# Performance work log

Measured on AMD Instinct MI355X. Metric: run time of the kernel, lower is better.

## Reference

```python
import jax, jax.numpy as jnp
import numpy as np

S, D, H, E = 4096, 1024, 16, 64  # seq_len, embed_dim, n_heads, head_size


def setup_inputs() -> dict:
    key = jax.random.key(0)
    ks = jax.random.split(key, 8)
    s_d = 1.0 / np.sqrt(D).astype(np.float32)
    return {
        "x": jax.random.normal(ks[0], (S, D), jnp.float32),
        # per-head Q/K/V projections (no bias), stacked over heads: [H, D, E]
        "Wk": jax.random.normal(ks[1], (H, D, E), jnp.float32) * s_d,
        "Wq": jax.random.normal(ks[2], (H, D, E), jnp.float32) * s_d,
        "Wv": jax.random.normal(ks[3], (H, D, E), jnp.float32) * s_d,
        # output projection Dense(D) with bias
        "Wo": jax.random.normal(ks[4], (H * E, D), jnp.float32) * (1.0 / np.sqrt(H * E).astype(np.float32)),
        "bo": jnp.zeros((D,), jnp.float32),
        # MLP: Dense(4D) -> gelu -> Dense(D), both with bias
        "W1": jax.random.normal(ks[5], (D, 4 * D), jnp.float32) * s_d,
        "b1": jnp.zeros((4 * D,), jnp.float32),
        "W2": jax.random.normal(ks[6], (4 * D, D), jnp.float32) * (1.0 / np.sqrt(4 * D).astype(np.float32)),
        "b2": jnp.zeros((D,), jnp.float32),
    }


def _attention(x, Wk, Wq, Wv):
    # per-head projections, vectorized over heads (original loops in Python)
    k = jnp.einsum('sd,hde->hse', x, Wk)
    q = jnp.einsum('sd,hde->hse', x, Wq)
    v = jnp.einsum('sd,hde->hse', x, Wv)
    # NOTE: original computes keys @ queries.T -> scores[i, j] = k_i . q_j
    scores = jnp.einsum('hse,hte->hst', k, q) / jnp.sqrt(jnp.float32(E))
    mask = jnp.tril(jnp.ones((x.shape[0], x.shape[0]), dtype=bool))  # [S, S]
    w = jax.nn.softmax(jnp.where(mask, scores, -jnp.inf), axis=-1)   # [H, S, S]
    out = jnp.einsum('hst,hte->hse', w, v)                            # [H, S, E]
    # concatenate heads along feature axis (head 0 first, matching the loop)
    return out.transpose(1, 0, 2).reshape(x.shape[0], -1)             # [S, H*E]


def reference(x, Wk, Wq, Wv, Wo, bo, W1, b1, W2, b2):
    x = x + _attention(x, Wk, Wq, Wv) @ Wo + bo
    h = jax.nn.gelu(x @ W1 + b1, approximate=True)  # flax default gelu (tanh approx)
    return x + h @ W2 + b2
```

## Files before the change

kernel.cpp:

```cpp
#include <hip/hip_runtime.h>

typedef __attribute__((ext_vector_type(8))) short s16x8;
typedef __attribute__((ext_vector_type(4))) short s16x4;
typedef __attribute__((ext_vector_type(4))) float f32x4;


__device__ __forceinline__ unsigned short f2bf(float f) {
    union { float f; unsigned u; } v; v.f = f;
    unsigned r = v.u + 0x7FFFu + ((v.u >> 16) & 1u);
    return (unsigned short)(r >> 16);
}

__device__ __forceinline__ float bf2f(unsigned short b) {
    union { unsigned u; float f; } v; v.u = ((unsigned)b) << 16;
    return v.f;
}

__device__ __forceinline__ unsigned cvt_pk_bf16(float lo, float hi) {
    unsigned r;
    asm("v_cvt_pk_bf16_f32 %0, %1, %2" : "=v"(r) : "v"(lo), "v"(hi));
    return r;
}

__device__ __forceinline__ float exp2_fast(float x) {
    float r;
    asm("v_exp_f32 %0, %1" : "=v"(r) : "v"(x));
    return r;
}

__device__ __forceinline__ float gelu_tanh(float x) {
    float u = 0.7978845608028654f * (x + 0.044715f * x * x * x);
    float au = fabsf(u);
    float t = 1.f - 2.f / (__expf(2.f * au) + 1.f);
    t = (u < 0.f) ? -t : t;
    return 0.5f * x * (1.f + t);
}

__device__ __forceinline__ void load_lds16(const void* g, void* l) {
    __builtin_amdgcn_global_load_lds(
        (const __attribute__((address_space(1))) void*)g,
        (__attribute__((address_space(3))) void*)l, 16, 0, 0);
}

__device__ __forceinline__ void xcd_remap(int& bx, int& by) {
    const int gx = gridDim.x;
    const int nwg = gx * gridDim.y;
    const int id = by * gx + bx;
    const int nid = (id & 7) * (nwg >> 3) + (id >> 3);
    bx = nid % gx; by = nid / gx;
}


__global__ void convert_bf16_k(const float* __restrict__ in,
                               unsigned short* __restrict__ out, int n) {
    int i = (blockIdx.x * blockDim.x + threadIdx.x) * 4;
    if (i >= n) return;
    float4 v = *(const float4*)(in + i);
    ushort4 o;
    o.x = f2bf(v.x); o.y = f2bf(v.y); o.z = f2bf(v.z); o.w = f2bf(v.w);
    *(ushort4*)(out + i) = o;
}

__global__ void transpose_k(const float* __restrict__ in,
                            unsigned short* __restrict__ out, int R, int C) {
    __shared__ float tile[32][33];
    const int b = blockIdx.z;
    const int c0 = blockIdx.x * 32, r0 = blockIdx.y * 32;
    const float* inb = in + (size_t)b * R * C;
    unsigned short* outb = out + (size_t)b * R * C;
    const int tx = threadIdx.x, ty = threadIdx.y;
    #pragma unroll
    for (int i = 0; i < 4; ++i)
        tile[ty + i*8][tx] = inb[(size_t)(r0 + ty + i*8) * C + c0 + tx];
    __syncthreads();
    #pragma unroll
    for (int i = 0; i < 4; ++i)
        outb[(size_t)(c0 + ty + i*8) * R + r0 + tx] = f2bf(tile[tx][ty + i*8]);
}

template<int EPI>
__global__ __launch_bounds__(256) void gemm_bt(
    const unsigned short* __restrict__ A,
    const unsigned short* __restrict__ BT,
    const float* __restrict__ bias,
    const float* __restrict__ resid,
    float* __restrict__ Cf,
    unsigned short* __restrict__ Cb,
    int M, int N, int K)
{
    __shared__ unsigned short As[3][128 * 32];
    __shared__ unsigned short Bs[3][128 * 32];
    const int tid = threadIdx.x;
    const int w  = tid >> 6, l = tid & 63;
    const int wr = w >> 1,  wc = w & 1;
    const int lg = l >> 4,  ll = l & 15;
    int bx = blockIdx.x, by = blockIdx.y;
    xcd_remap(bx, by);
    const int m0 = by * 128, n0 = bx * 128;

    const int srow = w * 16 + (l >> 2);
    const int scol = (((l & 3) ^ ((l >> 2) & 3))) * 8;

    f32x4 acc[4][4] = {};

    auto stage = [&](int buf, int k0) {
        #pragma unroll
        for (int i = 0; i < 2; ++i) {
            load_lds16(A  + (size_t)(m0 + srow + i*64) * K + k0 + scol,
                       (char*)As[buf] + i*4096 + w*1024);
            load_lds16(BT + (size_t)(n0 + srow + i*64) * K + k0 + scol,
                       (char*)Bs[buf] + i*4096 + w*1024);
        }
    };

    const int nsteps = K >> 5;
    stage(0, 0); stage(1, 32);
    int buf = 0;
    for (int s = 0; s < nsteps; ++s) {
        if (s + 1 < nsteps) asm volatile("s_waitcnt vmcnt(4)" ::: "memory");
        else                asm volatile("s_waitcnt vmcnt(0)" ::: "memory");
        __builtin_amdgcn_s_barrier();
        s16x8 a[4], b[4];
        #pragma unroll
        for (int m = 0; m < 4; ++m) {
            const int row = wr*64 + m*16 + ll;
            a[m] = *(const s16x8*)&As[buf][row * 32 + ((lg ^ (ll & 3)) * 8)];
        }
        #pragma unroll
        for (int n = 0; n < 4; ++n) {
            const int row = wc*64 + n*16 + ll;
            b[n] = *(const s16x8*)&Bs[buf][row * 32 + ((lg ^ (ll & 3)) * 8)];
        }
        int bnext = buf + 2; if (bnext >= 3) bnext -= 3;
        if (s + 2 < nsteps) stage(bnext, (s + 2) << 5);
        __builtin_amdgcn_s_setprio(1);
        #pragma unroll
        for (int m = 0; m < 4; ++m)
            #pragma unroll
            for (int n = 0; n < 4; ++n)
                acc[m][n] = __builtin_amdgcn_mfma_f32_16x16x32_bf16(a[m], b[n], acc[m][n], 0, 0, 0);
        __builtin_amdgcn_s_setprio(0);
        buf = (buf == 2) ? 0 : buf + 1;
    }

    #pragma unroll
    for (int m = 0; m < 4; ++m) {
        #pragma unroll
        for (int n = 0; n < 4; ++n) {
            const int col = n0 + wc*64 + n*16 + ll;
            #pragma unroll
            for (int r = 0; r < 4; ++r) {
                const int row = m0 + wr*64 + m*16 + lg*4 + r;
                float v = acc[m][n][r];
                if constexpr (EPI == 2) v = gelu_tanh(v + bias[col]);
                if constexpr (EPI == 4) v *= (col < 1024) ? 0.1803368801f : 1.0f;
                Cb[(size_t)row * N + col] = f2bf(v);
            }
        }
    }
}

template<int EPI>
__global__ __launch_bounds__(256) void gemm_bt64(
    const unsigned short* __restrict__ A,
    const unsigned short* __restrict__ BT,
    const float* __restrict__ bias,
    const float* __restrict__ resid,
    float* __restrict__ Cf,
    unsigned short* __restrict__ Cb,
    int M, int N, int K)
{
    __shared__ unsigned short As[4][128 * 32];
    __shared__ unsigned short Bs[4][64 * 32];
    const int tid = threadIdx.x;
    const int w  = tid >> 6, l = tid & 63;
    const int lg = l >> 4,  ll = l & 15;
    int bx = blockIdx.x, by = blockIdx.y;
    xcd_remap(bx, by);
    const int m0 = by * 128, n0 = bx * 64;

    const int srowA = w * 16 + (l >> 2);
    const int scolA = (((l & 3) ^ ((l >> 2) & 3))) * 8;
    const int srowB = tid >> 2;
    const int scolB = (((tid & 3) ^ ((tid >> 2) & 3))) * 8;

    f32x4 acc[2][4] = {};

    auto stage = [&](int buf, int k0) {
        #pragma unroll
        for (int i = 0; i < 2; ++i)
            load_lds16(A + (size_t)(m0 + srowA + i*64) * K + k0 + scolA,
                       (char*)As[buf] + i*4096 + w*1024);
        load_lds16(BT + (size_t)(n0 + srowB) * K + k0 + scolB,
                   (char*)Bs[buf] + w*1024);
    };

    const int nsteps = K >> 5;
    stage(0, 0); stage(1, 32); stage(2, 64);
    int buf = 0;
    for (int s = 0; s < nsteps; ++s) {
        const int rem = nsteps - 1 - s;
        if (rem >= 2)      asm volatile("s_waitcnt vmcnt(6)" ::: "memory");
        else if (rem == 1) asm volatile("s_waitcnt vmcnt(3)" ::: "memory");
        else               asm volatile("s_waitcnt vmcnt(0)" ::: "memory");
        __builtin_amdgcn_s_barrier();
        s16x8 a[2], b[4];
        #pragma unroll
        for (int m = 0; m < 2; ++m) {
            const int row = w*32 + m*16 + ll;
            a[m] = *(const s16x8*)&As[buf][row * 32 + ((lg ^ (ll & 3)) * 8)];
        }
        #pragma unroll
        for (int n = 0; n < 4; ++n) {
            const int row = n*16 + ll;
            b[n] = *(const s16x8*)&Bs[buf][row * 32 + ((lg ^ (ll & 3)) * 8)];
        }
        int bnext = buf + 3; if (bnext >= 4) bnext -= 4;
        if (s + 3 < nsteps) stage(bnext, (s + 3) << 5);
        __builtin_amdgcn_s_setprio(1);
        #pragma unroll
        for (int m = 0; m < 2; ++m)
            #pragma unroll
            for (int n = 0; n < 4; ++n)
                acc[m][n] = __builtin_amdgcn_mfma_f32_16x16x32_bf16(a[m], b[n], acc[m][n], 0, 0, 0);
        __builtin_amdgcn_s_setprio(0);
        buf = (buf + 1) & 3;
    }

    #pragma unroll
    for (int m = 0; m < 2; ++m) {
        #pragma unroll
        for (int n = 0; n < 4; ++n) {
            const int col = n0 + n*16 + ll;
            #pragma unroll
            for (int r = 0; r < 4; ++r) {
                const int row = m0 + w*32 + m*16 + lg*4 + r;
                float v = acc[m][n][r];
                if constexpr (EPI == 1 || EPI == 3) v += bias[col] + resid[(size_t)row * N + col];
                if constexpr (EPI != 3)
                    Cb[(size_t)row * N + col] = f2bf(v);
                if constexpr (EPI == 1 || EPI == 3)
                    Cf[(size_t)row * N + col] = v;
            }
        }
    }
}

__global__ __launch_bounds__(256) void attn_k(
    const unsigned short* __restrict__ Rq,
    const unsigned short* __restrict__ Ck,
    const unsigned short* __restrict__ Vt,
    unsigned short* __restrict__ Ppart,
    float* __restrict__ Lpart)
{
    __shared__ unsigned short Ks[3][64 * 64];
    __shared__ unsigned short Vs[3][64 * 64];

    const int bx = blockIdx.x;
    const int h  = bx & 15;
    const int j  = (bx >> 4) & 1;
    const int sb = 31 - (bx >> 5);
    const int t0 = j ? (sb + 1) : 0;
    const int t1 = j ? (2*sb + 2) : (sb + 1);

    const int tid = threadIdx.x;
    const int w = tid >> 6, l = tid & 63;
    const int lg = l >> 4, ll = l & 15;

    const int gsrc  = ((l & 7) ^ (l >> 3)) * 8;
    const int kOff0 = (w*16 +     (l >> 3)) * 2048 + h*64 + gsrc;
    const int kOff1 = (w*16 + 8 + (l >> 3)) * 2048 + h*64 + gsrc;
    const int vOff0 = (h*64 + w*16 +     (l >> 3)) * 4096 + gsrc;
    const int vOff1 = (h*64 + w*16 + 8 + (l >> 3)) * 4096 + gsrc;
    const int ldsOff = w * 2048;

    int qkoff[4][2];
    #pragma unroll
    for (int jj = 0; jj < 4; ++jj) {
        const int row = jj*16 + ll, r7 = row & 7;
        qkoff[jj][0] = row*128 + ((lg)     ^ r7) * 16;
        qkoff[jj][1] = row*128 + ((4 + lg) ^ r7) * 16;
    }
    int pvoff[4][2][2];
    #pragma unroll
    for (int n = 0; n < 4; ++n) {
        const int row = n*16 + ll, r7 = row & 7;
        #pragma unroll
        for (int c = 0; c < 2; ++c) {
            const int gl = (c*4     + (lg >> 1)) ^ r7;
            const int gh = (c*4 + 2 + (lg >> 1)) ^ r7;
            pvoff[n][c][0] = row*128 + gl*16 + (lg & 1)*8;
            pvoff[n][c][1] = row*128 + gh*16 + (lg & 1)*8;
        }
    }

    auto stage = [&](int t, int buf) {
        const unsigned short* qsrc = Ck + (size_t)t * 131072;
        const unsigned short* vsrc = Vt + t * 64;
        char* kd = (char*)Ks[buf] + ldsOff;
        char* vd = (char*)Vs[buf] + ldsOff;
        load_lds16(qsrc + kOff0, kd);
        load_lds16(qsrc + kOff1, kd + 1024);
        load_lds16(vsrc + vOff0, vd);
        load_lds16(vsrc + vOff1, vd + 1024);
    };

    const int row0 = sb*128 + w*32;
    const int qgA  = row0 + ll;
    const int qgB  = row0 + 16 + ll;
    const size_t rbA = (size_t)qgA * 2048 + h*64;
    const size_t rbB = (size_t)qgB * 2048 + h*64;
    const s16x8 rA0 = *(const s16x8*)&Rq[rbA + lg*8];
    const s16x8 rA1 = *(const s16x8*)&Rq[rbA + 32 + lg*8];
    const s16x8 rB0 = *(const s16x8*)&Rq[rbB + lg*8];
    const s16x8 rB1 = *(const s16x8*)&Rq[rbB + 32 + lg*8];

    const short onebf = (short)0x3F80;
    const s16x8 ones = {onebf, onebf, onebf, onebf, onebf, onebf, onebf, onebf};

    f32x4 o[2][4] = {};
    f32x4 o4[2] = {};

    stage(t0, 0);
    if (t0 + 1 < t1) stage(t0 + 1, 1);
    int buf = 0;

    for (int t = t0; t < t1; ++t) {
        if (t < t1-1) asm volatile("s_waitcnt vmcnt(4)" ::: "memory");
        else          asm volatile("s_waitcnt vmcnt(0)" ::: "memory");
        __builtin_amdgcn_s_barrier();
        const char* kb = (const char*)Ks[buf];
        const char* vb = (const char*)Vs[buf];
        const bool diag = (t >= 2*sb);

        f32x4 st[2][4];
        __builtin_amdgcn_s_setprio(1);
        #pragma unroll
        for (int jj = 0; jj < 4; ++jj) {
            s16x8 k0 = *(const s16x8*)(kb + qkoff[jj][0]);
            s16x8 k1 = *(const s16x8*)(kb + qkoff[jj][1]);
            f32x4 z = {0.f, 0.f, 0.f, 0.f};
            f32x4 ta = __builtin_amdgcn_mfma_f32_16x16x32_bf16(k0, rA0, z, 0, 0, 0);
            st[0][jj] = __builtin_amdgcn_mfma_f32_16x16x32_bf16(k1, rA1, ta, 0, 0, 0);
            f32x4 tb = __builtin_amdgcn_mfma_f32_16x16x32_bf16(k0, rB0, z, 0, 0, 0);
            st[1][jj] = __builtin_amdgcn_mfma_f32_16x16x32_bf16(k1, rB1, tb, 0, 0, 0);
        }
        __builtin_amdgcn_s_setprio(0);

        int bnext = buf + 2; if (bnext >= 3) bnext -= 3;
        if (t + 2 < t1) stage(t + 2, bnext);

        float p[2][4][4];
        if (diag) {
            #pragma unroll
            for (int jj = 0; jj < 4; ++jj)
                #pragma unroll
                for (int r = 0; r < 4; ++r) {
                    const int jg = t*64 + jj*16 + lg*4 + r;
                    p[0][jj][r] = exp2_fast((jg > qgA) ? -3e38f : st[0][jj][r]);
                    p[1][jj][r] = exp2_fast((jg > qgB) ? -3e38f : st[1][jj][r]);
                }
        } else {
            #pragma unroll
            for (int rs = 0; rs < 2; ++rs)
                #pragma unroll
                for (int jj = 0; jj < 4; ++jj)
                    #pragma unroll
                    for (int r = 0; r < 4; ++r)
                        p[rs][jj][r] = exp2_fast(st[rs][jj][r]);
        }

        s16x8 apv[2][2];
        #pragma unroll
        for (int rs = 0; rs < 2; ++rs)
            #pragma unroll
            for (int c = 0; c < 2; ++c) {
                union { unsigned u[4]; s16x8 v; } pk;
                pk.u[0] = cvt_pk_bf16(p[rs][2*c][0],   p[rs][2*c][1]);
                pk.u[1] = cvt_pk_bf16(p[rs][2*c][2],   p[rs][2*c][3]);
                pk.u[2] = cvt_pk_bf16(p[rs][2*c+1][0], p[rs][2*c+1][1]);
                pk.u[3] = cvt_pk_bf16(p[rs][2*c+1][2], p[rs][2*c+1][3]);
                apv[rs][c] = pk.v;
            }
        __builtin_amdgcn_s_setprio(1);
        #pragma unroll
        for (int rs = 0; rs < 2; ++rs) {
            o4[rs] = __builtin_amdgcn_mfma_f32_16x16x32_bf16(apv[rs][0], ones, o4[rs], 0, 0, 0);
            o4[rs] = __builtin_amdgcn_mfma_f32_16x16x32_bf16(apv[rs][1], ones, o4[rs], 0, 0, 0);
        }
        #pragma unroll
        for (int n = 0; n < 4; ++n) {
            #pragma unroll
            for (int c = 0; c < 2; ++c) {
                s16x4 lo = *(const s16x4*)(vb + pvoff[n][c][0]);
                s16x4 hi = *(const s16x4*)(vb + pvoff[n][c][1]);
                union { s16x4 h2[2]; s16x8 v; } u;
                u.h2[0] = lo; u.h2[1] = hi;
                o[0][n] = __builtin_amdgcn_mfma_f32_16x16x32_bf16(apv[0][c], u.v, o[0][n], 0, 0, 0);
                o[1][n] = __builtin_amdgcn_mfma_f32_16x16x32_bf16(apv[1][c], u.v, o[1][n], 0, 0, 0);
            }
        }
        __builtin_amdgcn_s_setprio(0);

        buf = (buf == 2) ? 0 : buf + 1;
    }

    unsigned short* Pout = Ppart + (size_t)j * 4194304;
    float* Lout = Lpart + (size_t)j * 65536;
    #pragma unroll
    for (int rs = 0; rs < 2; ++rs)
        #pragma unroll
        for (int r = 0; r < 4; ++r) {
            const int row = row0 + rs*16 + lg*4 + r;
            const size_t orow = (size_t)row * 1024 + h * 64;
            #pragma unroll
            for (int n = 0; n < 4; ++n)
                Pout[orow + n*16 + ll] = f2bf(o[rs][n][r]);
            if (ll == 0) Lout[row * 16 + h] = o4[rs][r];
        }
}

__global__ __launch_bounds__(256) void attn_combine_k(
    const unsigned short* __restrict__ P,
    const float* __restrict__ L,
    unsigned short* __restrict__ Out)
{
    const int idx = (blockIdx.x * 256 + threadIdx.x) * 4;
    const int row = idx >> 10, h = (idx & 1023) >> 6;
    const float inv = 1.f / (L[row*16 + h] + L[65536 + row*16 + h]);
    ushort4 a = *(const ushort4*)(P + idx);
    ushort4 b = *(const ushort4*)(P + 4194304 + idx);
    ushort4 o;
    o.x = f2bf((bf2f(a.x) + bf2f(b.x)) * inv);
    o.y = f2bf((bf2f(a.y) + bf2f(b.y)) * inv);
    o.z = f2bf((bf2f(a.z) + bf2f(b.z)) * inv);
    o.w = f2bf((bf2f(a.w) + bf2f(b.w)) * inv);
    *(ushort4*)(Out + idx) = o;
}


extern "C" void kernel_launch(void* const* d_in, const int* in_sizes, int n_in,
                              void* d_out, int out_size, void* d_ws, size_t ws_size,
                              hipStream_t stream) {
    const float* x  = (const float*)d_in[0];
    const float* Wk = (const float*)d_in[1];
    const float* Wq = (const float*)d_in[2];
    const float* Wv = (const float*)d_in[3];
    const float* Wo = (const float*)d_in[4];
    const float* bo = (const float*)d_in[5];
    const float* W1 = (const float*)d_in[6];
    const float* b1 = (const float*)d_in[7];
    const float* W2 = (const float*)d_in[8];
    const float* b2 = (const float*)d_in[9];
    float* out = (float*)d_out;

    char* ws = (char*)d_ws;
    unsigned short* x_bf  = (unsigned short*)(ws);
    unsigned short* WqkT  = (unsigned short*)(ws + (8u  << 20));
    unsigned short* WvT   = (unsigned short*)(ws + (12u << 20));
    unsigned short* WoT   = (unsigned short*)(ws + (14u << 20));
    unsigned short* W1T   = (unsigned short*)(ws + (16u << 20));
    unsigned short* W2T   = (unsigned short*)(ws + (24u << 20));
    unsigned short* QKm   = (unsigned short*)(ws + (32u << 20));
    unsigned short* attn  = (unsigned short*)(ws + (48u << 20));
    unsigned short* Vt    = (unsigned short*)(ws + (56u << 20));
    float*          yf    = (float*)(ws + (64u << 20));
    float*          Lpart = (float*)ws;
    unsigned short* Ppart = (unsigned short*)(ws + (64u << 20));
    unsigned short* y_bf  = x_bf;
    unsigned short* h_bf  = QKm;

    dim3 tb(32, 8);
    convert_bf16_k<<<4096, 256, 0, stream>>>(x, x_bf, 4096 * 1024);
    transpose_k<<<dim3(2, 32, 16),  tb, 0, stream>>>(Wq, WqkT,               1024, 64);
    transpose_k<<<dim3(2, 32, 16),  tb, 0, stream>>>(Wk, WqkT + 1024 * 1024, 1024, 64);
    transpose_k<<<dim3(2, 32, 16),  tb, 0, stream>>>(Wv, WvT, 1024, 64);
    transpose_k<<<dim3(32, 32, 1),  tb, 0, stream>>>(Wo, WoT, 1024, 1024);
    transpose_k<<<dim3(128, 32, 1), tb, 0, stream>>>(W1, W1T, 1024, 4096);
    transpose_k<<<dim3(32, 128, 1), tb, 0, stream>>>(W2, W2T, 4096, 1024);

    gemm_bt<4><<<dim3(16, 32), 256, 0, stream>>>(x_bf, WqkT, nullptr, nullptr, nullptr,
                                                 QKm, 4096, 2048, 1024);
    gemm_bt64<0><<<dim3(64, 8), 256, 0, stream>>>(WvT, x_bf, nullptr, nullptr, nullptr,
                                                  Vt, 1024, 4096, 1024);

    attn_k<<<1024, 256, 0, stream>>>(QKm + 1024 , QKm , Vt, Ppart, Lpart);
    attn_combine_k<<<4096, 256, 0, stream>>>(Ppart, Lpart, attn);

    gemm_bt64<1><<<dim3(16, 32), 256, 0, stream>>>(attn, WoT, bo, x, yf, y_bf, 4096, 1024, 1024);
    gemm_bt<2><<<dim3(32, 32),   256, 0, stream>>>(y_bf, W1T, b1, nullptr, nullptr, h_bf, 4096, 4096, 1024);
    gemm_bt64<3><<<dim3(16, 32), 256, 0, stream>>>(h_bf, W2T, b2, yf, out, nullptr, 4096, 1024, 4096);
}
```

Measured before the change: 251.8 us.

## Split-K the second MLP GEMM with 128x128 tiles plus a combine kernel

```diff
diff --git a/kernel.cpp b/kernel.cpp
--- a/kernel.cpp
+++ b/kernel.cpp
@@ -86,7 +86,7 @@
     const float* __restrict__ resid,
     float* __restrict__ Cf,
     unsigned short* __restrict__ Cb,
-    int M, int N, int K)
+    int M, int N, int K, int klen)
 {
     __shared__ unsigned short As[3][128 * 32];
     __shared__ unsigned short Bs[3][128 * 32];
@@ -97,6 +97,7 @@
     int bx = blockIdx.x, by = blockIdx.y;
     xcd_remap(bx, by);
     const int m0 = by * 128, n0 = bx * 128;
+    const int koff = (EPI == 5) ? (int)blockIdx.z * klen : 0;
 
     const int srow = w * 16 + (l >> 2);
     const int scol = (((l & 3) ^ ((l >> 2) & 3))) * 8;
@@ -106,14 +107,14 @@
     auto stage = [&](int buf, int k0) {
         #pragma unroll
         for (int i = 0; i < 2; ++i) {
-            load_lds16(A  + (size_t)(m0 + srow + i*64) * K + k0 + scol,
+            load_lds16(A  + (size_t)(m0 + srow + i*64) * K + koff + k0 + scol,
                        (char*)As[buf] + i*4096 + w*1024);
-            load_lds16(BT + (size_t)(n0 + srow + i*64) * K + k0 + scol,
+            load_lds16(BT + (size_t)(n0 + srow + i*64) * K + koff + k0 + scol,
                        (char*)Bs[buf] + i*4096 + w*1024);
         }
     };
 
-    const int nsteps = K >> 5;
+    const int nsteps = ((EPI == 5) ? klen : K) >> 5;
     stage(0, 0); stage(1, 32);
     int buf = 0;
     for (int s = 0; s < nsteps; ++s) {
@@ -143,6 +144,7 @@
         buf = (buf == 2) ? 0 : buf + 1;
     }
 
+    unsigned short* Cbz = (EPI == 5) ? (Cb + (size_t)blockIdx.z * M * N) : Cb;
     #pragma unroll
     for (int m = 0; m < 4; ++m) {
         #pragma unroll
@@ -154,7 +156,7 @@
                 float v = acc[m][n][r];
                 if constexpr (EPI == 2) v = gelu_tanh(v + bias[col]);
                 if constexpr (EPI == 4) v *= (col < 1024) ? 0.1803368801f : 1.0f;
-                Cb[(size_t)row * N + col] = f2bf(v);
+                Cbz[(size_t)row * N + col] = f2bf(v);
             }
         }
     }
@@ -236,14 +238,32 @@
             for (int r = 0; r < 4; ++r) {
                 const int row = m0 + w*32 + m*16 + lg*4 + r;
                 float v = acc[m][n][r];
-                if constexpr (EPI == 1 || EPI == 3) v += bias[col] + resid[(size_t)row * N + col];
-                if constexpr (EPI != 3)
-                    Cb[(size_t)row * N + col] = f2bf(v);
-                if constexpr (EPI == 1 || EPI == 3)
+                if constexpr (EPI == 1) v += bias[col] + resid[(size_t)row * N + col];
+                Cb[(size_t)row * N + col] = f2bf(v);
+                if constexpr (EPI == 1)
                     Cf[(size_t)row * N + col] = v;
             }
         }
     }
+}
+
+__global__ __launch_bounds__(256) void mlp2_combine_k(
+    const unsigned short* __restrict__ P,
+    const float* __restrict__ bias,
+    const float* __restrict__ resid,
+    float* __restrict__ out)
+{
+    const int idx = (blockIdx.x * 256 + threadIdx.x) * 4;
+    const int col = idx & 1023;
+    ushort4 a = *(const ushort4*)(P + idx);
+    ushort4 b = *(const ushort4*)(P + 4194304 + idx);
+    float4 rs = *(const float4*)(resid + idx);
+    float4 o;
+    o.x = bf2f(a.x) + bf2f(b.x) + bias[col]     + rs.x;
+    o.y = bf2f(a.y) + bf2f(b.y) + bias[col + 1] + rs.y;
+    o.z = bf2f(a.z) + bf2f(b.z) + bias[col + 2] + rs.z;
+    o.w = bf2f(a.w) + bf2f(b.w) + bias[col + 3] + rs.w;
+    *(float4*)(out + idx) = o;
 }
 
 __global__ __launch_bounds__(256) void attn_k(
@@ -467,6 +487,7 @@
     float*          yf    = (float*)(ws + (64u << 20));
     float*          Lpart = (float*)ws;
     unsigned short* Ppart = (unsigned short*)(ws + (64u << 20));
+    unsigned short* Pmlp  = (unsigned short*)(ws);
     unsigned short* y_bf  = x_bf;
     unsigned short* h_bf  = QKm;
 
@@ -480,14 +501,18 @@
     transpose_k<<<dim3(32, 128, 1), tb, 0, stream>>>(W2, W2T, 4096, 1024);
 
     gemm_bt<4><<<dim3(16, 32), 256, 0, stream>>>(x_bf, WqkT, nullptr, nullptr, nullptr,
-                                                 QKm, 4096, 2048, 1024);
+                                                 QKm, 4096, 2048, 1024, 1024);
     gemm_bt64<0><<<dim3(64, 8), 256, 0, stream>>>(WvT, x_bf, nullptr, nullptr, nullptr,
                                                   Vt, 1024, 4096, 1024);
 
     attn_k<<<1024, 256, 0, stream>>>(QKm + 1024 , QKm , Vt, Ppart, Lpart);
     attn_combine_k<<<4096, 256, 0, stream>>>(Ppart, Lpart, attn);
 
-    gemm_bt64<1><<<dim3(16, 32), 256, 0, stream>>>(attn, WoT, bo, x, yf, y_bf, 4096, 1024, 1024);
-    gemm_bt<2><<<dim3(32, 32),   256, 0, stream>>>(y_bf, W1T, b1, nullptr, nullptr, h_bf, 4096, 4096, 1024);
-    gemm_bt64<3><<<dim3(16, 32), 256, 0, stream>>>(h_bf, W2T, b2, yf, out, nullptr, 4096, 1024, 4096);
-}
+    gemm_bt64<1><<<dim3(16, 32), 256, 0, stream>>>(attn, WoT, bo, x, yf, y_bf,
+                                                   4096, 1024, 1024);
+    gemm_bt<2><<<dim3(32, 32), 256, 0, stream>>>(y_bf, W1T, b1, nullptr, nullptr, h_bf,
+                                                 4096, 4096, 1024, 1024);
+    gemm_bt<5><<<dim3(8, 32, 2), 256, 0, stream>>>(h_bf, W2T, nullptr, nullptr, nullptr,
+                                                   Pmlp, 4096, 1024, 4096, 2048);
+    mlp2_combine_k<<<4096, 256, 0, stream>>>(Pmlp, b2, yf, out);
+}
```

Result: no change. 249.1 us (-1.1%).
